# Optimization experiments

Measured on AMD Instinct MI355X. Metric: run time of the kernel, lower is better.

Reference implementation:

```python
import jax, jax.numpy as jnp
import numpy as np

WINDOW = 64
BAND_NUM = 2 * WINDOW      # 128
FILTER_LEN = 6 * WINDOW    # 384


def setup_inputs() -> dict:
    key = jax.random.key(0)
    k1, k2 = jax.random.split(key)
    B, C, T, F = 16, 1, 8192, WINDOW + 1  # F = band_num/2 + 1 = 65
    inp = jax.random.normal(k1, (B, C, T, F), dtype=jnp.float32)
    subband_filter = jax.random.normal(k2, (FILTER_LEN,), dtype=jnp.float32)
    lengths = jnp.full((B,), T, dtype=jnp.int32)  # one sample per batch element, all length T
    return {"input": inp, "subband_filter": subband_filter, "lengths": lengths}


def reference(input, subband_filter, lengths):
    B, C, T, F = input.shape
    S = lengths.shape[0]               # sample_num (static)
    x = input.reshape(-1, F)           # (N, F), N = B*C*T
    # torch.fft.irfft(norm='forward') -> jnp.fft.irfft(norm='forward'), out len = 2*(F-1) = band_num
    ifft_out = jnp.fft.irfft(x, norm='forward')          # (N, 128)
    # tile across the 3 band repeats, apply prototype filter and window gain
    wide = jnp.concatenate([ifft_out, ifft_out, ifft_out], axis=1)  # (N, 384)
    wide = wide * subband_filter[None, :] * WINDOW
    N = wide.shape[0]
    H = N // S                          # in_height (= C*T per sample)
    w = wide.reshape(S, H, 6, WINDOW)   # per-sample, per-frame, 6 taps of width `window`
    true_len = H - 5
    # overlap-add: out[s, t] = sum_k w[s, t + 5 - k, k]
    out = w[:, 5:H, 0, :]
    for k in range(1, 6):
        out = out + w[:, 5 - k:H - k, k, :]
    out = out.reshape(B, C, -1)         # (B, C, true_len*window)
    return out / 32768.0
```

## Files before the change

### kernel.cpp

```cpp
#include <hip/hip_runtime.h>
#include <hip/hip_bf16.h>


#define NF 65
#define NT 8192
#define TRUE_LEN 8187
#define FPW 59
#define WPB 139
#define TAB_STRIDE 68
#define YS_STRIDE 66

typedef const __attribute__((address_space(4))) float cfloat;
typedef float v2f __attribute__((ext_vector_type(2)));

__device__ float d_tab[33 * TAB_STRIDE];

__global__ void build_tab_kernel() {
    int idx = blockIdx.x * 256 + threadIdx.x;
    if (idx >= 33 * TAB_STRIDE) return;
    int p = idx / TAB_STRIDE, n = idx % TAB_STRIDE;
    if (n == 33 || n >= 66) { d_tab[idx] = 0.0f; return; }
    int m = (n < 33) ? 2 * n : 2 * (n - 34) + 1;
    float w = (m == 0 || m == 64) ? 1.0f : 2.0f;
    int a = (m * p) & 127;
    d_tab[idx] = w * cospif((float)a * (1.0f / 64.0f));
}

__global__ __launch_bounds__(256)
void subband_main_kernel(const float* __restrict__ g_in,
                         const float* __restrict__ g_filt,
                         float* __restrict__ g_out)
{
    __shared__ __hip_bfloat16 Ys[4][64 * YS_STRIDE];

    const int tid  = threadIdx.x;
    const int lane = tid & 63;
    const int wv   = tid >> 6;
    const int wg   = blockIdx.x * 4 + wv;
    const int s     = wg / WPB;
    const int fbase = (wg % WPB) * FPW;
    int h = fbase + lane;
    if (h > NT - 1) h = NT - 1;

    const float* xr = g_in + ((size_t)s * NT + h) * NF;
    v2f Xe[17], Xo[16];
    #pragma unroll
    for (int c = 0; c < 16; ++c) {
        float t4[4];
        __builtin_memcpy(t4, xr + 4 * c, 16);
        Xe[c] = (v2f){t4[0], t4[2]};
        Xo[c] = (v2f){t4[1], t4[3]};
    }
    Xe[16] = (v2f){xr[64], 0.0f};

    __hip_bfloat16* ys = &Ys[wv][0];
    cfloat* ct = (cfloat*)(unsigned long long)(const float*)d_tab;

    for (int p = 0; p < 33; ++p) {
        cfloat* cf = ct + p * TAB_STRIDE;
        v2f aE = (v2f){0.0f, 0.0f}, aO = (v2f){0.0f, 0.0f};
        #pragma unroll
        for (int k = 0; k < 16; ++k) {
            v2f ce, co;
            __builtin_memcpy(&ce, cf + 2 * k, 8);
            __builtin_memcpy(&co, cf + 34 + 2 * k, 8);
            aE = __builtin_elementwise_fma(ce, Xe[k], aE);
            aO = __builtin_elementwise_fma(co, Xo[k], aO);
        }
        {
            v2f ce;
            __builtin_memcpy(&ce, cf + 32, 8);
            aE = __builtin_elementwise_fma(ce, Xe[16], aE);
        }
        const float e = aE.x + aE.y, o = aO.x + aO.y;
        ys[lane * YS_STRIDE + p]      = __float2bfloat16(e + o);
        ys[lane * YS_STRIDE + 64 - p] = __float2bfloat16(e - o);
    }

    const int j = lane;
    float fc[6];
    #pragma unroll
    for (int k = 0; k < 6; ++k) fc[k] = g_filt[k * 64 + j] * (1.0f / 512.0f);
    const int te = j;
    const int to = (j == 0) ? 64 : 64 - j;

    float we[6], wo[6];
    #pragma unroll
    for (int r = 0; r < 5; ++r) {
        we[r] = __bfloat162float(ys[r * YS_STRIDE + te]);
        wo[r] = __bfloat162float(ys[r * YS_STRIDE + to]);
    }
    float* dst = g_out + ((size_t)s * TRUE_LEN + fbase) * 64 + j;

    #pragma unroll
    for (int q = 0; q < FPW; ++q) {
        if (fbase + q >= TRUE_LEN) break;
        we[5] = __bfloat162float(ys[(q + 5) * YS_STRIDE + te]);
        wo[5] = __bfloat162float(ys[(q + 5) * YS_STRIDE + to]);
        const float o = fc[0] * we[5] + fc[1] * wo[4] + fc[2] * we[3]
                      + fc[3] * wo[2] + fc[4] * we[1] + fc[5] * wo[0];
        dst[(size_t)q * 64] = o;
        #pragma unroll
        for (int r = 0; r < 5; ++r) { we[r] = we[r + 1]; wo[r] = wo[r + 1]; }
    }
}

extern "C" void kernel_launch(void* const* d_in, const int* in_sizes, int n_in,
                              void* d_out, int out_size, void* d_ws, size_t ws_size,
                              hipStream_t stream) {
    const float* g_in   = (const float*)d_in[0];
    const float* g_filt = (const float*)d_in[1];
    float* g_out = (float*)d_out;

    build_tab_kernel<<<9, 256, 0, stream>>>();
    subband_main_kernel<<<556, 256, 0, stream>>>(g_in, g_filt, g_out);
}
```

Measured before the change: 99.19 us.

## Stage input rows through LDS with coalesced global_load_lds and cache twiddle table

Each wave now copies its contiguous block of input rows into LDS with coalesced 16-byte global_load_lds transfers. Lanes then read their 65-float rows from LDS instead of each lane issuing strided global loads. The staging buffer is reused as the bf16 overlap-add scratch, and blocks shrink to 128 threads with twice as many blocks. The cosine table kernel becomes a single block that returns early once a ready flag is set, so the table is built only once across calls. The trade-off is a larger LDS footprint per wave, which may limit occupancy.

```diff
diff --git a/kernel.cpp b/kernel.cpp
--- a/kernel.cpp
+++ b/kernel.cpp
@@ -9,51 +9,79 @@
 #define WPB 139
 #define TAB_STRIDE 68
 #define YS_STRIDE 66
+#define XSTG 4352
 
 typedef const __attribute__((address_space(4))) float cfloat;
+typedef const __attribute__((address_space(1))) void gvoid;
+typedef __attribute__((address_space(3))) void lvoid;
 typedef float v2f __attribute__((ext_vector_type(2)));
 
 __device__ float d_tab[33 * TAB_STRIDE];
+__device__ int d_tab_ready;
 
 __global__ void build_tab_kernel() {
-    int idx = blockIdx.x * 256 + threadIdx.x;
-    if (idx >= 33 * TAB_STRIDE) return;
-    int p = idx / TAB_STRIDE, n = idx % TAB_STRIDE;
-    if (n == 33 || n >= 66) { d_tab[idx] = 0.0f; return; }
-    int m = (n < 33) ? 2 * n : 2 * (n - 34) + 1;
-    float w = (m == 0 || m == 64) ? 1.0f : 2.0f;
-    int a = (m * p) & 127;
-    d_tab[idx] = w * cospif((float)a * (1.0f / 64.0f));
+    if (d_tab_ready) return;
+    for (int idx = threadIdx.x; idx < 33 * TAB_STRIDE; idx += 256) {
+        int p = idx / TAB_STRIDE, n = idx % TAB_STRIDE;
+        float v = 0.0f;
+        if (n < 66 && n != 33) {
+            int m = (n < 33) ? 2 * n : 2 * (n - 34) + 1;
+            float w = (m == 0 || m == 64) ? 1.0f : 2.0f;
+            int a = (m * p) & 127;
+            v = w * cospif((float)a * (1.0f / 64.0f));
+        }
+        d_tab[idx] = v;
+    }
+    __syncthreads();
+    if (threadIdx.x == 0) d_tab_ready = 1;
 }
 
-__global__ __launch_bounds__(256)
+__global__ __launch_bounds__(128)
 void subband_main_kernel(const float* __restrict__ g_in,
                          const float* __restrict__ g_filt,
                          float* __restrict__ g_out)
 {
-    __shared__ __hip_bfloat16 Ys[4][64 * YS_STRIDE];
+    __shared__ __align__(16) float Xs[2][XSTG];
 
     const int tid  = threadIdx.x;
     const int lane = tid & 63;
     const int wv   = tid >> 6;
-    const int wg   = blockIdx.x * 4 + wv;
+    const int wg   = blockIdx.x * 2 + wv;
     const int s     = wg / WPB;
     const int fbase = (wg % WPB) * FPW;
-    int h = fbase + lane;
-    if (h > NT - 1) h = NT - 1;
 
-    const float* xr = g_in + ((size_t)s * NT + h) * NF;
+    const size_t row0_f = ((size_t)s * NT + fbase) * NF;
+    const size_t base_f = row0_f & ~(size_t)3;
+    const int    delta  = (int)(row0_f - base_f);
+    const float* gsrc   = g_in + base_f;
+    const float* gend   = g_in + ((size_t)16 * NT * NF - 4);
+
+    float* xs = &Xs[wv][0];
+    #pragma unroll
+    for (int c = 0; c < 17; ++c) {
+        const float* src = gsrc + c * 256 + lane * 4;
+        if (src > gend) src = gend;
+        __builtin_amdgcn_global_load_lds((gvoid*)src, (lvoid*)(xs + c * 256),
+                                         16, 0, 0);
+    }
+    asm volatile("s_waitcnt vmcnt(0)" ::: "memory");
+
+    const int rb = delta + lane * NF;
+    float X[NF];
+    #pragma unroll
+    for (int c = 0; c < NF; ++c) X[c] = xs[rb + c];
+
     v2f Xe[17], Xo[16];
     #pragma unroll
     for (int c = 0; c < 16; ++c) {
-        float t4[4];
-        __builtin_memcpy(t4, xr + 4 * c, 16);
-        Xe[c] = (v2f){t4[0], t4[2]};
-        Xo[c] = (v2f){t4[1], t4[3]};
+        Xe[c] = (v2f){X[4 * c + 0], X[4 * c + 2]};
+        Xo[c] = (v2f){X[4 * c + 1], X[4 * c + 3]};
     }
-    Xe[16] = (v2f){xr[64], 0.0f};
+    Xe[16] = (v2f){X[64], 0.0f};
 
-    __hip_bfloat16* ys = &Ys[wv][0];
+    asm volatile("" ::: "memory");
+
+    __hip_bfloat16* ys = (__hip_bfloat16*)xs;
     cfloat* ct = (cfloat*)(unsigned long long)(const float*)d_tab;
 
     for (int p = 0; p < 33; ++p) {
@@ -112,6 +140,6 @@
     const float* g_filt = (const float*)d_in[1];
     float* g_out = (float*)d_out;
 
-    build_tab_kernel<<<9, 256, 0, stream>>>();
-    subband_main_kernel<<<556, 256, 0, stream>>>(g_in, g_filt, g_out);
+    build_tab_kernel<<<1, 256, 0, stream>>>();
+    subband_main_kernel<<<1112, 128, 0, stream>>>(g_in, g_filt, g_out);
 }
```

After: 109.3 us. 10.1% more time.
